# Performance work log

Measured on AMD Instinct MI355X. Metric: run time of the kernel, lower is better.

The kernel has to match this reference:

```python
import jax, jax.numpy as jnp
import numpy as np

A = 5          # angRes
C = 128        # channels
SPA = 2 * C    # spa_dim
NH = 8         # num_heads
KW = 11        # mask_field[1]


def setup_inputs() -> dict:
    key = jax.random.key(0)
    ks = jax.random.split(key, 12)
    s = 0.05
    return {
        "buffer": jax.random.normal(ks[0], (2, C, A * A, 32, 32), jnp.float32),
        "Win": jax.random.normal(ks[1], (SPA, C), jnp.float32) * s,
        "ln_w": jnp.ones((SPA,), jnp.float32),
        "ln_b": jnp.zeros((SPA,), jnp.float32),
        "in_proj": jax.random.normal(ks[2], (3 * SPA, SPA), jnp.float32) * s,
        "attn_out_w": jax.random.normal(ks[3], (SPA, SPA), jnp.float32) * s,
        "ffn_ln_w": jnp.ones((SPA,), jnp.float32),
        "ffn_ln_b": jnp.zeros((SPA,), jnp.float32),
        "ff1": jax.random.normal(ks[4], (2 * SPA, SPA), jnp.float32) * s,
        "ff2": jax.random.normal(ks[5], (SPA, 2 * SPA), jnp.float32) * s,
        "Wout": jax.random.normal(ks[6], (C, SPA), jnp.float32) * s,
        "conv_w": jax.random.normal(ks[7], (C, C, 1, 3, 3), jnp.float32) * s,
    }


def layer_norm(x, w, b, eps=1e-5):
    mu = x.mean(-1, keepdims=True)
    var = ((x - mu) ** 2).mean(-1, keepdims=True)
    return (x - mu) * jax.lax.rsqrt(var + eps) * w + b


def gen_mask(h, w, k_h, k_w):
    # additive mask over flattened (h*w) x (h*w) grid, local window k_h x k_w
    i = jnp.arange(h)
    j = jnp.arange(w)
    mh = (i[None, :] >= i[:, None] - k_h // 2) & (i[None, :] < i[:, None] + (k_h - k_h // 2))
    mw = (j[None, :] >= j[:, None] - k_w // 2) & (j[None, :] < j[:, None] + (k_w - k_w // 2))
    allowed = (mh[:, None, :, None] & mw[None, :, None, :]).reshape(h * w, h * w)
    return jnp.where(allowed, 0.0, -jnp.inf)


def basic_trans(x, Win, ln_w, ln_b, in_proj, attn_out_w,
                ffn_ln_w, ffn_ln_b, ff1, ff2, Wout):
    b, c, n, v, w = x.shape
    mask = gen_mask(v, w, 2 * A, KW)                       # (L, L)
    # 'b c n v w -> (v w) (b n) c'
    tok = x.transpose(3, 4, 0, 2, 1).reshape(v * w, b * n, c)
    tok = tok @ Win.T                                       # (L, B, E)
    tn = layer_norm(tok, ln_w, ln_b)
    L, B, E = tok.shape
    hd = E // NH
    Wq, Wk, Wv = jnp.split(in_proj, 3, axis=0)
    q = (tn @ Wq.T).reshape(L, B, NH, hd)
    k = (tn @ Wk.T).reshape(L, B, NH, hd)
    vv = (tok @ Wv.T).reshape(L, B, NH, hd)                 # value = un-normed tok
    scores = jnp.einsum('lbhd,mbhd->bhlm', q, k) / np.float32(np.sqrt(hd))
    scores = scores + mask[None, None]
    attn = jax.nn.softmax(scores, axis=-1)
    o = jnp.einsum('bhlm,mbhd->lbhd', attn, vv).reshape(L, B, E)
    tok = o @ attn_out_w.T + tok
    ff = layer_norm(tok, ffn_ln_w, ffn_ln_b)
    ff = jax.nn.relu(ff @ ff1.T) @ ff2.T
    tok = ff + tok
    tok = tok @ Wout.T                                      # (L, B, c)
    # '(v w) (b n) c -> b c n v w'
    return tok.reshape(v, w, b, n, c).transpose(2, 4, 3, 0, 1)


def reference(buffer, Win, ln_w, ln_b, in_proj, attn_out_w,
              ffn_ln_w, ffn_ln_b, ff1, ff2, Wout, conv_w):
    a = A
    b, c, uv, h, w = buffer.shape
    bt = lambda z: basic_trans(z, Win, ln_w, ln_b, in_proj, attn_out_w,
                               ffn_ln_w, ffn_ln_b, ff1, ff2, Wout)
    conv = lambda z: jax.lax.conv_general_dilated(
        z, conv_w, (1, 1, 1), ((0, 0), (1, 1), (1, 1)),
        dimension_numbers=('NCDHW', 'OIDHW', 'NCDHW'))

    # pass 1: 'b c (u v) h w -> b c (v w) u h'
    x = buffer.reshape(b, c, a, a, h, w).transpose(0, 1, 3, 5, 2, 4).reshape(b, c, a * w, a, h)
    x = bt(x)
    x = x.reshape(b, c, a, w, a, h).transpose(0, 1, 4, 2, 5, 3).reshape(b, c, a * a, h, w)
    x = conv(x) + buffer
    sc2 = x
    # pass 2: 'b c (u v) h w -> b c (u h) v w'
    y = x.reshape(b, c, a, a, h, w).transpose(0, 1, 2, 4, 3, 5).reshape(b, c, a * h, a, w)
    y = bt(y)
    y = y.reshape(b, c, a, h, a, w).transpose(0, 1, 2, 4, 3, 5).reshape(b, c, a * a, h, w)
    return conv(y) + sc2
```

## Files before the change

kernel.cpp:

```cpp
#include <hip/hip_runtime.h>
#include <math.h>
#include <stdint.h>

typedef __attribute__((ext_vector_type(8))) short bf16x8;
typedef __attribute__((ext_vector_type(4))) float f32x4;

static __device__ __forceinline__ unsigned short f2bf(float f) {
    unsigned u = __builtin_bit_cast(unsigned, f);
    unsigned r = u + 0x7fffu + ((u >> 16) & 1u);
    return (unsigned short)(r >> 16);
}
static __device__ __forceinline__ float bf2f(unsigned short h) {
    return __builtin_bit_cast(float, ((unsigned)h) << 16);
}
static __device__ __forceinline__ void gload_lds16(const void* g, void* l) {
    __builtin_amdgcn_global_load_lds((const __attribute__((address_space(1))) unsigned int*)g,
                                     (__attribute__((address_space(3))) unsigned int*)l, 16, 0, 0);
}

__global__ __launch_bounds__(256) void gather1(const float* __restrict__ src,
                                               unsigned short* __restrict__ x0, int W, int bb0) {
    int cct = blockIdx.x & 3, y = blockIdx.x >> 2;
    int n = blockIdx.y; int u = n / 5, v = n % 5;
    int lb = blockIdx.z, bb = bb0 + lb;
    __shared__ float tile[32][33];
    int tx = threadIdx.x & 31, tg = threadIdx.x >> 5;
    const float* s = src + (((size_t)(bb * 128 + cct * 32) * 25 + n) * 32 + y) * 32;
    #pragma unroll
    for (int i = 0; i < 4; i++) {
        int cl = tg + 8 * i;
        tile[cl][tx] = s[(size_t)cl * 25600 + tx];
    }
    __syncthreads();
    unsigned short* d = x0 + ((size_t)(u * 32 + y) * W + lb * 160 + v * 32) * 128 + cct * 32;
    #pragma unroll
    for (int i = 0; i < 4; i++) {
        int xx = tg + 8 * i;
        d[(size_t)xx * 128 + tx] = f2bf(tile[tx][xx]);
    }
}

__global__ __launch_bounds__(256) void gather2(const float* __restrict__ src,
                                               unsigned short* __restrict__ x0, int W, int bb0) {
    int cct = blockIdx.x & 3, x = blockIdx.x >> 2;
    int n = blockIdx.y; int u = n / 5, v = n % 5;
    int lb = blockIdx.z, bb = bb0 + lb;
    __shared__ float tile[32][33];
    int tx = threadIdx.x & 31, tg = threadIdx.x >> 5;
    const float* s = src + (((size_t)(bb * 128 + cct * 32) * 25 + n) * 32) * 32 + x;
    #pragma unroll
    for (int i = 0; i < 4; i++) {
        int cl = tg + 8 * i;
        tile[cl][tx] = s[(size_t)cl * 25600 + tx * 32];
    }
    __syncthreads();
    unsigned short* d = x0 + ((size_t)(v * 32 + x) * W + lb * 160 + u * 32) * 128 + cct * 32;
    #pragma unroll
    for (int i = 0; i < 4; i++) {
        int yy = tg + 8 * i;
        d[(size_t)yy * 128 + tx] = f2bf(tile[tx][yy]);
    }
}

__global__ __launch_bounds__(256) void repack_w(const float* __restrict__ cw,
                                                unsigned short* __restrict__ wb) {
    int g = blockIdx.x * 256 + threadIdx.x;
    int co = g / 1152;
    int rem = g - co * 1152;
    int ci = rem / 9, tap = rem - ci * 9;
    wb[((size_t)tap * 128 + co) * 128 + ci] = f2bf(cw[g]);
}

__global__ __launch_bounds__(256) void conv_weights(const float* __restrict__ Win,
                                                    const float* __restrict__ in_proj,
                                                    const float* __restrict__ attn_out_w,
                                                    const float* __restrict__ ff1,
                                                    const float* __restrict__ ff2,
                                                    const float* __restrict__ Wout,
                                                    unsigned short* __restrict__ wg) {
    int g = blockIdx.x * 256 + threadIdx.x;
    float v;
    if      (g < 32768)  v = Win[g];
    else if (g < 229376) v = in_proj[g - 32768];
    else if (g < 294912) v = attn_out_w[g - 229376];
    else if (g < 425984) v = ff1[g - 294912];
    else if (g < 557056) v = ff2[g - 425984];
    else                 v = Wout[g - 557056];
    wg[g] = f2bf(v);
}

__global__ __launch_bounds__(256) void ln_bf16(const unsigned short* __restrict__ in,
                                               unsigned short* __restrict__ out,
                                               const float* __restrict__ w, const float* __restrict__ b) {
    int tok = blockIdx.x * 4 + (threadIdx.x >> 6);
    int lane = threadIdx.x & 63;
    ushort4 h4 = ((const ushort4*)(in + (size_t)tok * 256))[lane];
    float vx = bf2f(h4.x), vy = bf2f(h4.y), vz = bf2f(h4.z), vw = bf2f(h4.w);
    float s = vx + vy + vz + vw;
    #pragma unroll
    for (int off = 32; off > 0; off >>= 1) s += __shfl_xor(s, off);
    float mu = s * (1.0f / 256.0f);
    float dx = vx - mu, dy = vy - mu, dz = vz - mu, dw = vw - mu;
    float vs = dx * dx + dy * dy + dz * dz + dw * dw;
    #pragma unroll
    for (int off = 32; off > 0; off >>= 1) vs += __shfl_xor(vs, off);
    float inv = rsqrtf(vs * (1.0f / 256.0f) + 1e-5f);
    float4 wv = ((const float4*)w)[lane];
    float4 bv = ((const float4*)b)[lane];
    ushort4 o4;
    o4.x = f2bf(dx * inv * wv.x + bv.x);
    o4.y = f2bf(dy * inv * wv.y + bv.y);
    o4.z = f2bf(dz * inv * wv.z + bv.z);
    o4.w = f2bf(dw * inv * wv.w + bv.w);
    *(ushort4*)(out + (size_t)tok * 256 + lane * 4) = o4;
}

static __device__ __forceinline__ void gemm_core(const unsigned short* __restrict__ X,
                                                 const unsigned short* __restrict__ Wt,
                                                 int bm, int bnrow, int K,
                                                 unsigned short (&As)[2][128 * 32],
                                                 unsigned short (&Bs)[2][128 * 32],
                                                 f32x4 (&acc)[4][4]) {
    const int tid = threadIdx.x;
    const int lane = tid & 63, w = tid >> 6;
    const int wm = (w >> 1) * 64, wn = (w & 1) * 64;
    const int lr = lane & 15, lq = lane >> 4;
    #pragma unroll
    for (int m = 0; m < 4; m++)
        #pragma unroll
        for (int n = 0; n < 4; n++)
            acc[m][n] = (f32x4){0.f, 0.f, 0.f, 0.f};

    const int srow = lane >> 2, sslot = lane & 3;
    auto STAGE = [&](int bsel, int k0) {
        #pragma unroll
        for (int c = 0; c < 2; ++c) {
            int row = (w << 5) + (c << 4) + srow;
            int sl = sslot ^ (row & 3);
            gload_lds16(X  + (size_t)(bm + row) * K + k0 + sl * 8,
                        &As[bsel][(w << 10) + (c << 9)]);
            gload_lds16(Wt + (size_t)(bnrow + row) * K + k0 + sl * 8,
                        &Bs[bsel][(w << 10) + (c << 9)]);
        }
    };

    const int nt = K >> 5;
    STAGE(0, 0);
    __syncthreads();
    int cur = 0;
    for (int t = 0; t < nt; ++t) {
        if (t + 1 < nt) STAGE(cur ^ 1, (t + 1) << 5);
        const char* Ab = (const char*)As[cur];
        const char* Bb = (const char*)Bs[cur];
        bf16x8 af[4], bf[4];
        #pragma unroll
        for (int m = 0; m < 4; m++) {
            int row = wm + m * 16 + lr;
            af[m] = *(const bf16x8*)(Ab + row * 64 + ((lq * 16) ^ ((row & 3) << 4)));
        }
        #pragma unroll
        for (int n = 0; n < 4; n++) {
            int row = wn + n * 16 + lr;
            bf[n] = *(const bf16x8*)(Bb + row * 64 + ((lq * 16) ^ ((row & 3) << 4)));
        }
        #pragma unroll
        for (int m = 0; m < 4; m++)
            #pragma unroll
            for (int n = 0; n < 4; n++)
                acc[m][n] = __builtin_amdgcn_mfma_f32_16x16x32_bf16(af[m], bf[n], acc[m][n], 0, 0, 0);
        if (t + 1 < nt) __syncthreads();
        cur ^= 1;
    }
}

__global__ __launch_bounds__(256) void gemm_bf16(const unsigned short* __restrict__ X,
                                                 const unsigned short* __restrict__ Wt,
                                                 unsigned short* __restrict__ Yb,
                                                 const unsigned short* __restrict__ Rb,
                                                 int N, int K, int relu, int spass, int W) {
    __shared__ unsigned short As[2][128 * 32];
    __shared__ unsigned short Bs[2][128 * 32];
    const int bm = blockIdx.x * 128, bn = blockIdx.y * 128;
    f32x4 acc[4][4];
    gemm_core(X, Wt, bm, bn, K, As, Bs, acc);

    const int lane = threadIdx.x & 63, w = threadIdx.x >> 6;
    const int wm = (w >> 1) * 64, wn = (w & 1) * 64;
    const int lr = lane & 15, lq = lane >> 4;
    #pragma unroll
    for (int m = 0; m < 4; m++) {
        #pragma unroll
        for (int r = 0; r < 4; r++) {
            int row = bm + wm + m * 16 + lq * 4 + r;
            size_t base;
            if (spass == 0) {
                base = (size_t)row * N;
            } else {
                int l = row / W, c = row - l * W;
                int lb = (c >= 160) ? 1 : 0, sp = c - lb * 160;
                int sl_, pix;
                if (spass == 1) { int u = l >> 5, y = l & 31, v = sp >> 5, x = sp & 31;
                                  sl_ = lb * 25 + u * 5 + v; pix = y * 32 + x; }
                else            { int v = l >> 5, x = l & 31, u = sp >> 5, y = sp & 31;
                                  sl_ = lb * 25 + u * 5 + v; pix = y * 32 + x; }
                base = ((size_t)sl_ * 1024 + pix) * 128;
            }
            #pragma unroll
            for (int n = 0; n < 4; n++) {
                int col = bn + wn + n * 16 + lr;
                float val = acc[m][n][r];
                if (Rb) val += bf2f(Rb[(size_t)row * N + col]);
                if (relu) val = fmaxf(val, 0.0f);
                Yb[base + col] = f2bf(val);
            }
        }
    }
}

__global__ __launch_bounds__(256) void gemm_qkv(const unsigned short* __restrict__ tn,
                                                const unsigned short* __restrict__ tok,
                                                const unsigned short* __restrict__ Wqkv,
                                                unsigned short* __restrict__ QK,
                                                unsigned short* __restrict__ V) {
    __shared__ unsigned short As[2][128 * 32];
    __shared__ unsigned short Bs[2][128 * 32];
    const int bm = blockIdx.x * 128, by = blockIdx.y;
    const unsigned short* X = (by < 4) ? tn : tok;
    f32x4 acc[4][4];
    gemm_core(X, Wqkv, bm, by * 128, 256, As, Bs, acc);

    unsigned short* Yb = (by < 4) ? QK : V;
    const int N = (by < 4) ? 512 : 256;
    const int bn = (by < 4) ? by * 128 : (by - 4) * 128;
    const int lane = threadIdx.x & 63, w = threadIdx.x >> 6;
    const int wm = (w >> 1) * 64, wn = (w & 1) * 64;
    const int lr = lane & 15, lq = lane >> 4;
    #pragma unroll
    for (int m = 0; m < 4; m++) {
        #pragma unroll
        for (int r = 0; r < 4; r++) {
            int row = bm + wm + m * 16 + lq * 4 + r;
            #pragma unroll
            for (int n = 0; n < 4; n++) {
                int col = bn + wn + n * 16 + lr;
                Yb[(size_t)row * N + col] = f2bf(acc[m][n][r]);
            }
        }
    }
}

__global__ __launch_bounds__(256) void vtrans(const unsigned short* __restrict__ vtok,
                                              unsigned short* __restrict__ vt, int W) {
    const int col = blockIdx.x, h = blockIdx.y;
    __shared__ unsigned short t[160][34];
    const int tid = threadIdx.x;
    for (int i = tid; i < 160 * 16; i += 256) {
        int l = i >> 4, dp = i & 15;
        unsigned v = *(const unsigned*)(vtok + ((size_t)l * W + col) * 256 + h * 32 + dp * 2);
        *(unsigned*)&t[l][dp * 2] = v;
    }
    __syncthreads();
    unsigned short* dst = vt + (((size_t)h * W + col) * 32) * 160;
    for (int i = tid; i < 32 * 160; i += 256) {
        int d = i / 160, l = i - d * 160;
        dst[i] = t[l][d];
    }
}

__global__ __launch_bounds__(64) void attn_mfma(const unsigned short* __restrict__ qk,
                                                const unsigned short* __restrict__ vt,
                                                unsigned short* __restrict__ o, int W) {
    const int col = blockIdx.x;
    const int h = blockIdx.y;
    const int lane = threadIdx.x;
    const int lr = lane & 15, lq = lane >> 4;
    __shared__ __align__(16) unsigned short P_lds[16][168];

    bf16x8 kf[10];
    #pragma unroll
    for (int m = 0; m < 10; m++) {
        size_t t = (size_t)(m * 16 + lr) * W + col;
        kf[m] = *(const bf16x8*)(qk + t * 512 + 256 + h * 32 + lq * 8);
    }
    const unsigned short* vbase = vt + (((size_t)h * W + col) * 32) * 160;
    bf16x8 vf[2][5];
    #pragma unroll
    for (int md = 0; md < 2; md++)
        #pragma unroll
        for (int c = 0; c < 5; c++)
            vf[md][c] = *(const bf16x8*)(vbase + (size_t)(md * 16 + lr) * 160 + c * 32 + lq * 8);

    const float scale = 0.17677669529663687f;
    for (int n = 0; n < 10; n++) {
        const int q = n * 16 + lr;
        bf16x8 qf = *(const bf16x8*)(qk + ((size_t)q * W + col) * 512 + h * 32 + lq * 8);
        f32x4 p[10];
        #pragma unroll
        for (int m = 0; m < 10; m++)
            p[m] = __builtin_amdgcn_mfma_f32_16x16x32_bf16(kf[m], qf, (f32x4){0.f,0.f,0.f,0.f}, 0, 0, 0);
        const int b = lq * 4 - ((n & 1) * 16 + lr);
        float mx = -1e30f;
        #pragma unroll
        for (int m = 0; m < 10; m++) {
            #pragma unroll
            for (int r = 0; r < 4; r++) {
                int dd = b + (m & 1) * 16 + r;
                float s = ((unsigned)(dd + 5) <= 10u) ? p[m][r] : -1e30f;
                p[m][r] = s;
                mx = fmaxf(mx, s);
            }
        }
        mx = fmaxf(mx, __shfl_xor(mx, 16));
        mx = fmaxf(mx, __shfl_xor(mx, 32));
        float sum = 0.f;
        #pragma unroll
        for (int m = 0; m < 10; m++) {
            #pragma unroll
            for (int r = 0; r < 4; r++) {
                float e = __expf((p[m][r] - mx) * scale);
                p[m][r] = e;
                sum += e;
            }
        }
        sum += __shfl_xor(sum, 16);
        sum += __shfl_xor(sum, 32);
        #pragma unroll
        for (int m = 0; m < 10; m++) {
            ushort4 pk;
            pk.x = f2bf(p[m][0]); pk.y = f2bf(p[m][1]);
            pk.z = f2bf(p[m][2]); pk.w = f2bf(p[m][3]);
            *(ushort4*)&P_lds[lr][m * 16 + lq * 4] = pk;
        }
        f32x4 oa0 = (f32x4){0.f,0.f,0.f,0.f}, oa1 = (f32x4){0.f,0.f,0.f,0.f};
        #pragma unroll
        for (int c = 0; c < 5; c++) {
            bf16x8 pf = *(const bf16x8*)&P_lds[lr][c * 32 + lq * 8];
            oa0 = __builtin_amdgcn_mfma_f32_16x16x32_bf16(vf[0][c], pf, oa0, 0, 0, 0);
            oa1 = __builtin_amdgcn_mfma_f32_16x16x32_bf16(vf[1][c], pf, oa1, 0, 0, 0);
        }
        const float inv = 1.0f / sum;
        unsigned short* op = o + ((size_t)q * W + col) * 256 + h * 32;
        ushort4 s0, s1;
        s0.x = f2bf(oa0[0] * inv); s0.y = f2bf(oa0[1] * inv);
        s0.z = f2bf(oa0[2] * inv); s0.w = f2bf(oa0[3] * inv);
        s1.x = f2bf(oa1[0] * inv); s1.y = f2bf(oa1[1] * inv);
        s1.z = f2bf(oa1[2] * inv); s1.w = f2bf(oa1[3] * inv);
        *(ushort4*)(op + lq * 4)      = s0;
        *(ushort4*)(op + 16 + lq * 4) = s1;
    }
}

__global__ __launch_bounds__(256) void conv_mfma(const unsigned short* __restrict__ xp,
                                                 const unsigned short* __restrict__ wb,
                                                 const float* __restrict__ res,
                                                 float* __restrict__ out, int bb0) {
    const int ptile = blockIdx.x;
    const int slice = blockIdx.y;
    const int lb = slice / 25, n = slice % 25;
    const int bb = bb0 + lb;
    const int y0 = ptile * 4;
    __shared__ unsigned short As[128 * 64];
    __shared__ unsigned short Bs[128 * 64];
    const int tid = threadIdx.x;
    const int lane = tid & 63, w = tid >> 6;
    const int wm = (w >> 1) * 64;
    const int wn = (w & 1) * 64;
    const int lr = lane & 15, lq = lane >> 4;
    const unsigned short* xs = xp + (size_t)slice * 1024 * 128;
    f32x4 acc[4][4];
    #pragma unroll
    for (int m = 0; m < 4; m++)
        #pragma unroll
        for (int nn = 0; nn < 4; nn++)
            acc[m][nn] = (f32x4){0.f, 0.f, 0.f, 0.f};

    for (int tap = 0; tap < 9; tap++) {
        const int dy = tap / 3 - 1, dx = tap % 3 - 1;
        for (int c0 = 0; c0 < 128; c0 += 64) {
            #pragma unroll
            for (int i = 0; i < 4; i++) {
                int id = tid + 256 * i;
                int row = id >> 3, cg = id & 7;
                int py = y0 + (row >> 5) + dy;
                int px = (row & 31) + dx;
                uint4 v = {0u, 0u, 0u, 0u};
                if ((unsigned)py < 32u && (unsigned)px < 32u)
                    v = *(const uint4*)(xs + ((size_t)(py * 32 + px) * 128 + c0 + cg * 8));
                int boff = row * 128 + ((cg * 16) ^ ((row & 7) << 4));
                *(uint4*)((char*)As + boff) = v;
            }
            #pragma unroll
            for (int i = 0; i < 4; i++) {
                int id = tid + 256 * i;
                int row = id >> 3, cg = id & 7;
                uint4 v = *(const uint4*)(wb + (((size_t)tap * 128 + row) * 128 + c0 + cg * 8));
                int boff = row * 128 + ((cg * 16) ^ ((row & 7) << 4));
                *(uint4*)((char*)Bs + boff) = v;
            }
            __syncthreads();
            #pragma unroll
            for (int ks = 0; ks < 2; ks++) {
                bf16x8 wf[4], xf[4];
                #pragma unroll
                for (int m = 0; m < 4; m++) {
                    int row = wm + m * 16 + lr;
                    int boff = row * 128 + ((ks * 64 + lq * 16) ^ ((row & 7) << 4));
                    wf[m] = *(const bf16x8*)((const char*)Bs + boff);
                }
                #pragma unroll
                for (int nn = 0; nn < 4; nn++) {
                    int row = wn + nn * 16 + lr;
                    int boff = row * 128 + ((ks * 64 + lq * 16) ^ ((row & 7) << 4));
                    xf[nn] = *(const bf16x8*)((const char*)As + boff);
                }
                #pragma unroll
                for (int m = 0; m < 4; m++)
                    #pragma unroll
                    for (int nn = 0; nn < 4; nn++)
                        acc[m][nn] = __builtin_amdgcn_mfma_f32_16x16x32_bf16(wf[m], xf[nn], acc[m][nn], 0, 0, 0);
            }
            __syncthreads();
        }
    }
    #pragma unroll
    for (int m = 0; m < 4; m++) {
        int co0 = wm + m * 16 + lq * 4;
        #pragma unroll
        for (int r = 0; r < 4; r++) {
            size_t rowoff = (((size_t)(bb * 128 + co0 + r) * 25 + n) * 1024) + ptile * 128;
            #pragma unroll
            for (int nn = 0; nn < 4; nn++) {
                int pix = wn + nn * 16 + lr;
                out[rowoff + pix] = acc[m][nn][r] + res[rowoff + pix];
            }
        }
    }
}

extern "C" void kernel_launch(void* const* d_in, const int* in_sizes, int n_in,
                              void* d_out, int out_size, void* d_ws, size_t ws_size,
                              hipStream_t stream) {
    (void)in_sizes; (void)n_in; (void)out_size;
    const float* buffer     = (const float*)d_in[0];
    const float* Win        = (const float*)d_in[1];
    const float* ln_w       = (const float*)d_in[2];
    const float* ln_b       = (const float*)d_in[3];
    const float* in_proj    = (const float*)d_in[4];
    const float* attn_out_w = (const float*)d_in[5];
    const float* ffn_ln_w   = (const float*)d_in[6];
    const float* ffn_ln_b   = (const float*)d_in[7];
    const float* ff1        = (const float*)d_in[8];
    const float* ff2        = (const float*)d_in[9];
    const float* Wout       = (const float*)d_in[10];
    const float* conv_w     = (const float*)d_in[11];
    float* out = (float*)d_out;
    float* ws  = (float*)d_ws;

    const size_t need2 = ((size_t)51200 * 960 + 368640) * 4;
    int NBB = (ws_size >= need2) ? 2 : 1;
    const int W = NBB * 160;
    const size_t T = (size_t)NBB * 25600;

    unsigned short* x0b   = (unsigned short*)ws;
    unsigned short* Abf   = (unsigned short*)(ws + T * 64);
    unsigned short* tnb   = (unsigned short*)(ws + T * 192);
    float*          C     = ws + T * 320;
    unsigned short* QKtok = (unsigned short*)C;
    unsigned short* Vtok  = (unsigned short*)(C + T * 256);
    unsigned short* Vt    = (unsigned short*)(C + T * 384);
    unsigned short* hidb  = (unsigned short*)C;
    unsigned short* xp    = (unsigned short*)C;
    unsigned short* Db    = (unsigned short*)(ws + T * 832);
    unsigned short* wg    = (unsigned short*)(ws + T * 960);
    unsigned short* wb    = (unsigned short*)(ws + T * 960 + 294912);

    const unsigned short* Winb  = wg;
    const unsigned short* Wqkvb = wg + 32768;
    const unsigned short* Waob  = wg + 229376;
    const unsigned short* Wff1b = wg + 294912;
    const unsigned short* Wff2b = wg + 425984;
    const unsigned short* Woutb = wg + 557056;

    const int GM = (int)(T / 128);

    conv_weights<<<2304, 256, 0, stream>>>(Win, in_proj, attn_out_w, ff1, ff2, Wout, wg);
    repack_w<<<576, 256, 0, stream>>>(conv_w, wb);

    for (int pass = 0; pass < 2; pass++) {
        const float* src = (pass == 0) ? buffer : out;
        for (int bb0 = 0; bb0 < 2; bb0 += NBB) {
            if (pass == 0) gather1<<<dim3(128, 25, NBB), 256, 0, stream>>>(src, x0b, W, bb0);
            else           gather2<<<dim3(128, 25, NBB), 256, 0, stream>>>(src, x0b, W, bb0);

            gemm_bf16<<<dim3(GM, 2), 256, 0, stream>>>(x0b, Winb, Abf, nullptr, 256, 128, 0, 0, W);
            ln_bf16<<<(int)(T / 4), 256, 0, stream>>>(Abf, tnb, ln_w, ln_b);
            gemm_qkv<<<dim3(GM, 6), 256, 0, stream>>>(tnb, Abf, Wqkvb, QKtok, Vtok);
            vtrans<<<dim3(W, 8), 256, 0, stream>>>(Vtok, Vt, W);
            attn_mfma<<<dim3(W, 8), 64, 0, stream>>>(QKtok, Vt, Db, W);
            gemm_bf16<<<dim3(GM, 2), 256, 0, stream>>>(Db, Waob, Abf, Abf, 256, 256, 0, 0, W);
            ln_bf16<<<(int)(T / 4), 256, 0, stream>>>(Abf, tnb, ffn_ln_w, ffn_ln_b);
            gemm_bf16<<<dim3(GM, 4), 256, 0, stream>>>(tnb, Wff1b, hidb, nullptr, 512, 256, 1, 0, W);
            gemm_bf16<<<dim3(GM, 2), 256, 0, stream>>>(hidb, Wff2b, Abf, Abf, 256, 512, 0, 0, W);
            gemm_bf16<<<dim3(GM, 1), 256, 0, stream>>>(Abf, Woutb, xp, nullptr, 128, 256, 0, pass + 1, W);

            conv_mfma<<<dim3(8, NBB * 25), 256, 0, stream>>>(
                xp, wb, (pass == 0) ? buffer : (const float*)out, out, bb0);
        }
    }
}
```

Baseline: 658.6 us.

## Triple-buffer GEMM LDS staging and fuse V transpose into QKV epilogue

The shared GEMM core moves from double to triple buffering. It issues loads two k-tiles ahead and waits with explicit vmcnt counters plus raw barriers instead of __syncthreads. The LDS swizzle pattern changes from row&3 to (row>>1)&3 to cut bank conflicts on the fragment reads. The separate vtrans kernel is removed: the QKV GEMM epilogue writes V straight into the transposed per-head layout. That saves one launch and one round trip of V through memory, at the cost of scattered 2-byte stores and more LDS per block, which may lower occupancy.

```diff
diff --git a/kernel.cpp b/kernel.cpp
--- a/kernel.cpp
+++ b/kernel.cpp
@@ -118,8 +118,8 @@
 static __device__ __forceinline__ void gemm_core(const unsigned short* __restrict__ X,
                                                  const unsigned short* __restrict__ Wt,
                                                  int bm, int bnrow, int K,
-                                                 unsigned short (&As)[2][128 * 32],
-                                                 unsigned short (&Bs)[2][128 * 32],
+                                                 unsigned short (&As)[3][128 * 32],
+                                                 unsigned short (&Bs)[3][128 * 32],
                                                  f32x4 (&acc)[4][4]) {
     const int tid = threadIdx.x;
     const int lane = tid & 63, w = tid >> 6;
@@ -136,7 +136,7 @@
         #pragma unroll
         for (int c = 0; c < 2; ++c) {
             int row = (w << 5) + (c << 4) + srow;
-            int sl = sslot ^ (row & 3);
+            int sl = sslot ^ ((row >> 1) & 3);
             gload_lds16(X  + (size_t)(bm + row) * K + k0 + sl * 8,
                         &As[bsel][(w << 10) + (c << 9)]);
             gload_lds16(Wt + (size_t)(bnrow + row) * K + k0 + sl * 8,
@@ -146,30 +146,36 @@
 
     const int nt = K >> 5;
     STAGE(0, 0);
-    __syncthreads();
-    int cur = 0;
+    STAGE(1, 32);
+    asm volatile("s_waitcnt vmcnt(4)" ::: "memory");
+    __builtin_amdgcn_s_barrier();
+    __builtin_amdgcn_sched_barrier(0);
     for (int t = 0; t < nt; ++t) {
-        if (t + 1 < nt) STAGE(cur ^ 1, (t + 1) << 5);
-        const char* Ab = (const char*)As[cur];
-        const char* Bb = (const char*)Bs[cur];
+        if (t + 2 < nt) STAGE((t + 2) % 3, (t + 2) << 5);
+        const char* Ab = (const char*)As[t % 3];
+        const char* Bb = (const char*)Bs[t % 3];
         bf16x8 af[4], bf[4];
         #pragma unroll
         for (int m = 0; m < 4; m++) {
             int row = wm + m * 16 + lr;
-            af[m] = *(const bf16x8*)(Ab + row * 64 + ((lq * 16) ^ ((row & 3) << 4)));
+            af[m] = *(const bf16x8*)(Ab + row * 64 + ((lq * 16) ^ (((row >> 1) & 3) << 4)));
         }
         #pragma unroll
         for (int n = 0; n < 4; n++) {
             int row = wn + n * 16 + lr;
-            bf[n] = *(const bf16x8*)(Bb + row * 64 + ((lq * 16) ^ ((row & 3) << 4)));
+            bf[n] = *(const bf16x8*)(Bb + row * 64 + ((lq * 16) ^ (((row >> 1) & 3) << 4)));
         }
         #pragma unroll
         for (int m = 0; m < 4; m++)
             #pragma unroll
             for (int n = 0; n < 4; n++)
                 acc[m][n] = __builtin_amdgcn_mfma_f32_16x16x32_bf16(af[m], bf[n], acc[m][n], 0, 0, 0);
-        if (t + 1 < nt) __syncthreads();
-        cur ^= 1;
+        if (t + 1 < nt) {
+            if (t + 2 < nt) asm volatile("s_waitcnt vmcnt(4)" ::: "memory");
+            else            asm volatile("s_waitcnt vmcnt(0)" ::: "memory");
+            __builtin_amdgcn_s_barrier();
+            __builtin_amdgcn_sched_barrier(0);
+        }
     }
 }
 
@@ -178,8 +184,8 @@
                                                  unsigned short* __restrict__ Yb,
                                                  const unsigned short* __restrict__ Rb,
                                                  int N, int K, int relu, int spass, int W) {
-    __shared__ unsigned short As[2][128 * 32];
-    __shared__ unsigned short Bs[2][128 * 32];
+    __shared__ unsigned short As[3][128 * 32];
+    __shared__ unsigned short Bs[3][128 * 32];
     const int bm = blockIdx.x * 128, bn = blockIdx.y * 128;
     f32x4 acc[4][4];
     gemm_core(X, Wt, bm, bn, K, As, Bs, acc);
@@ -221,49 +227,46 @@
                                                 const unsigned short* __restrict__ tok,
                                                 const unsigned short* __restrict__ Wqkv,
                                                 unsigned short* __restrict__ QK,
-                                                unsigned short* __restrict__ V) {
-    __shared__ unsigned short As[2][128 * 32];
-    __shared__ unsigned short Bs[2][128 * 32];
+                                                unsigned short* __restrict__ Vt, int W) {
+    __shared__ unsigned short As[3][128 * 32];
+    __shared__ unsigned short Bs[3][128 * 32];
     const int bm = blockIdx.x * 128, by = blockIdx.y;
     const unsigned short* X = (by < 4) ? tn : tok;
     f32x4 acc[4][4];
     gemm_core(X, Wqkv, bm, by * 128, 256, As, Bs, acc);
 
-    unsigned short* Yb = (by < 4) ? QK : V;
-    const int N = (by < 4) ? 512 : 256;
-    const int bn = (by < 4) ? by * 128 : (by - 4) * 128;
     const int lane = threadIdx.x & 63, w = threadIdx.x >> 6;
     const int wm = (w >> 1) * 64, wn = (w & 1) * 64;
     const int lr = lane & 15, lq = lane >> 4;
-    #pragma unroll
-    for (int m = 0; m < 4; m++) {
-        #pragma unroll
-        for (int r = 0; r < 4; r++) {
-            int row = bm + wm + m * 16 + lq * 4 + r;
-            #pragma unroll
-            for (int n = 0; n < 4; n++) {
-                int col = bn + wn + n * 16 + lr;
-                Yb[(size_t)row * N + col] = f2bf(acc[m][n][r]);
-            }
-        }
-    }
-}
-
-__global__ __launch_bounds__(256) void vtrans(const unsigned short* __restrict__ vtok,
-                                              unsigned short* __restrict__ vt, int W) {
-    const int col = blockIdx.x, h = blockIdx.y;
-    __shared__ unsigned short t[160][34];
-    const int tid = threadIdx.x;
-    for (int i = tid; i < 160 * 16; i += 256) {
-        int l = i >> 4, dp = i & 15;
-        unsigned v = *(const unsigned*)(vtok + ((size_t)l * W + col) * 256 + h * 32 + dp * 2);
-        *(unsigned*)&t[l][dp * 2] = v;
-    }
-    __syncthreads();
-    unsigned short* dst = vt + (((size_t)h * W + col) * 32) * 160;
-    for (int i = tid; i < 32 * 160; i += 256) {
-        int d = i / 160, l = i - d * 160;
-        dst[i] = t[l][d];
+    if (by < 4) {
+        const int bn = by * 128;
+        #pragma unroll
+        for (int m = 0; m < 4; m++) {
+            #pragma unroll
+            for (int r = 0; r < 4; r++) {
+                int row = bm + wm + m * 16 + lq * 4 + r;
+                #pragma unroll
+                for (int n = 0; n < 4; n++) {
+                    int col = bn + wn + n * 16 + lr;
+                    QK[(size_t)row * 512 + col] = f2bf(acc[m][n][r]);
+                }
+            }
+        }
+    } else {
+        #pragma unroll
+        for (int m = 0; m < 4; m++) {
+            #pragma unroll
+            for (int r = 0; r < 4; r++) {
+                int row = bm + wm + m * 16 + lq * 4 + r;
+                int l = row / W, c = row - l * W;
+                #pragma unroll
+                for (int n = 0; n < 4; n++) {
+                    int vr = (by - 4) * 128 + wn + n * 16 + lr;
+                    int h = vr >> 5, d = vr & 31;
+                    Vt[(((size_t)h * W + c) * 32 + d) * 160 + l] = f2bf(acc[m][n][r]);
+                }
+            }
+        }
     }
 }
 
@@ -466,7 +469,6 @@
     unsigned short* tnb   = (unsigned short*)(ws + T * 192);
     float*          C     = ws + T * 320;
     unsigned short* QKtok = (unsigned short*)C;
-    unsigned short* Vtok  = (unsigned short*)(C + T * 256);
     unsigned short* Vt    = (unsigned short*)(C + T * 384);
     unsigned short* hidb  = (unsigned short*)C;
     unsigned short* xp    = (unsigned short*)C;
@@ -494,8 +496,7 @@
 
             gemm_bf16<<<dim3(GM, 2), 256, 0, stream>>>(x0b, Winb, Abf, nullptr, 256, 128, 0, 0, W);
             ln_bf16<<<(int)(T / 4), 256, 0, stream>>>(Abf, tnb, ln_w, ln_b);
-            gemm_qkv<<<dim3(GM, 6), 256, 0, stream>>>(tnb, Abf, Wqkvb, QKtok, Vtok);
-            vtrans<<<dim3(W, 8), 256, 0, stream>>>(Vtok, Vt, W);
+            gemm_qkv<<<dim3(GM, 6), 256, 0, stream>>>(tnb, Abf, Wqkvb, QKtok, Vt, W);
             attn_mfma<<<dim3(W, 8), 64, 0, stream>>>(QKtok, Vt, Db, W);
             gemm_bf16<<<dim3(GM, 2), 256, 0, stream>>>(Db, Waob, Abf, Abf, 256, 256, 0, 0, W);
             ln_bf16<<<(int)(T / 4), 256, 0, stream>>>(Abf, tnb, ffn_ln_w, ffn_ln_b);
```

New measurement: 807.1 us. +22.6%, slower.

## Shrink GEMM tiles to 64x64 and remap blocks across XCDs

Applied to the files above, without the earlier changes.

Replaces the 128x128 GEMM tile core with a 64x64 variant, where each wave computes a 32x32 sub-tile and all 256 threads issue one LDS load each per operand. The LDS swizzle pattern is adjusted to match. A block-index remap groups consecutive M tiles onto the same XCD so they share L2 reuse of the weights and activations. Grids grow fourfold to give the 256 CUs more blocks to keep busy. The cost is less data reuse per block and lower MFMA density per wave.

```diff
diff --git a/kernel.cpp b/kernel.cpp
--- a/kernel.cpp
+++ b/kernel.cpp
@@ -115,33 +115,39 @@
     *(ushort4*)(out + (size_t)tok * 256 + lane * 4) = o4;
 }
 
-static __device__ __forceinline__ void gemm_core(const unsigned short* __restrict__ X,
-                                                 const unsigned short* __restrict__ Wt,
-                                                 int bm, int bnrow, int K,
-                                                 unsigned short (&As)[2][128 * 32],
-                                                 unsigned short (&Bs)[2][128 * 32],
-                                                 f32x4 (&acc)[4][4]) {
+static __device__ __forceinline__ void xcd_remap(int& bxi, int& byi) {
+    int d = blockIdx.x + gridDim.x * blockIdx.y;
+    int s = d & 7;
+    unsigned j = (unsigned)(d >> 3);
+    unsigned ny = gridDim.y;
+    int gm8 = (int)(gridDim.x >> 3);
+    bxi = s * gm8 + (int)(j / ny);
+    byi = (int)(j % ny);
+}
+
+static __device__ __forceinline__ void gemm_core64(const unsigned short* __restrict__ X,
+                                                   const unsigned short* __restrict__ Wt,
+                                                   int bm, int bnrow, int K,
+                                                   unsigned short (&As)[2][64 * 32],
+                                                   unsigned short (&Bs)[2][64 * 32],
+                                                   f32x4 (&acc)[2][2]) {
     const int tid = threadIdx.x;
     const int lane = tid & 63, w = tid >> 6;
-    const int wm = (w >> 1) * 64, wn = (w & 1) * 64;
+    const int wm = (w >> 1) * 32, wn = (w & 1) * 32;
     const int lr = lane & 15, lq = lane >> 4;
     #pragma unroll
-    for (int m = 0; m < 4; m++)
-        #pragma unroll
-        for (int n = 0; n < 4; n++)
+    for (int m = 0; m < 2; m++)
+        #pragma unroll
+        for (int n = 0; n < 2; n++)
             acc[m][n] = (f32x4){0.f, 0.f, 0.f, 0.f};
 
-    const int srow = lane >> 2, sslot = lane & 3;
+    const int srow = tid >> 2, sslot = tid & 3;
+    const int ssl = sslot ^ ((srow >> 1) & 3);
     auto STAGE = [&](int bsel, int k0) {
-        #pragma unroll
-        for (int c = 0; c < 2; ++c) {
-            int row = (w << 5) + (c << 4) + srow;
-            int sl = sslot ^ (row & 3);
-            gload_lds16(X  + (size_t)(bm + row) * K + k0 + sl * 8,
-                        &As[bsel][(w << 10) + (c << 9)]);
-            gload_lds16(Wt + (size_t)(bnrow + row) * K + k0 + sl * 8,
-                        &Bs[bsel][(w << 10) + (c << 9)]);
-        }
+        gload_lds16(X  + (size_t)(bm + srow) * K + k0 + ssl * 8,
+                    &As[bsel][tid * 8]);
+        gload_lds16(Wt + (size_t)(bnrow + srow) * K + k0 + ssl * 8,
+                    &Bs[bsel][tid * 8]);
     };
 
     const int nt = K >> 5;
@@ -152,21 +158,21 @@
         if (t + 1 < nt) STAGE(cur ^ 1, (t + 1) << 5);
         const char* Ab = (const char*)As[cur];
         const char* Bb = (const char*)Bs[cur];
-        bf16x8 af[4], bf[4];
-        #pragma unroll
-        for (int m = 0; m < 4; m++) {
+        bf16x8 af[2], bf[2];
+        #pragma unroll
+        for (int m = 0; m < 2; m++) {
             int row = wm + m * 16 + lr;
-            af[m] = *(const bf16x8*)(Ab + row * 64 + ((lq * 16) ^ ((row & 3) << 4)));
-        }
-        #pragma unroll
-        for (int n = 0; n < 4; n++) {
+            af[m] = *(const bf16x8*)(Ab + row * 64 + ((lq * 16) ^ (((row >> 1) & 3) << 4)));
+        }
+        #pragma unroll
+        for (int n = 0; n < 2; n++) {
             int row = wn + n * 16 + lr;
-            bf[n] = *(const bf16x8*)(Bb + row * 64 + ((lq * 16) ^ ((row & 3) << 4)));
-        }
-        #pragma unroll
-        for (int m = 0; m < 4; m++)
-            #pragma unroll
-            for (int n = 0; n < 4; n++)
+            bf[n] = *(const bf16x8*)(Bb + row * 64 + ((lq * 16) ^ (((row >> 1) & 3) << 4)));
+        }
+        #pragma unroll
+        for (int m = 0; m < 2; m++)
+            #pragma unroll
+            for (int n = 0; n < 2; n++)
                 acc[m][n] = __builtin_amdgcn_mfma_f32_16x16x32_bf16(af[m], bf[n], acc[m][n], 0, 0, 0);
         if (t + 1 < nt) __syncthreads();
         cur ^= 1;
@@ -178,17 +184,19 @@
                                                  unsigned short* __restrict__ Yb,
                                                  const unsigned short* __restrict__ Rb,
                                                  int N, int K, int relu, int spass, int W) {
-    __shared__ unsigned short As[2][128 * 32];
-    __shared__ unsigned short Bs[2][128 * 32];
-    const int bm = blockIdx.x * 128, bn = blockIdx.y * 128;
-    f32x4 acc[4][4];
-    gemm_core(X, Wt, bm, bn, K, As, Bs, acc);
+    __shared__ unsigned short As[2][64 * 32];
+    __shared__ unsigned short Bs[2][64 * 32];
+    int bxi, byi;
+    xcd_remap(bxi, byi);
+    const int bm = bxi * 64, bn = byi * 64;
+    f32x4 acc[2][2];
+    gemm_core64(X, Wt, bm, bn, K, As, Bs, acc);
 
     const int lane = threadIdx.x & 63, w = threadIdx.x >> 6;
-    const int wm = (w >> 1) * 64, wn = (w & 1) * 64;
+    const int wm = (w >> 1) * 32, wn = (w & 1) * 32;
     const int lr = lane & 15, lq = lane >> 4;
     #pragma unroll
-    for (int m = 0; m < 4; m++) {
+    for (int m = 0; m < 2; m++) {
         #pragma unroll
         for (int r = 0; r < 4; r++) {
             int row = bm + wm + m * 16 + lq * 4 + r;
@@ -206,7 +214,7 @@
                 base = ((size_t)sl_ * 1024 + pix) * 128;
             }
             #pragma unroll
-            for (int n = 0; n < 4; n++) {
+            for (int n = 0; n < 2; n++) {
                 int col = bn + wn + n * 16 + lr;
                 float val = acc[m][n][r];
                 if (Rb) val += bf2f(Rb[(size_t)row * N + col]);
@@ -222,26 +230,28 @@
                                                 const unsigned short* __restrict__ Wqkv,
                                                 unsigned short* __restrict__ QK,
                                                 unsigned short* __restrict__ V) {
-    __shared__ unsigned short As[2][128 * 32];
-    __shared__ unsigned short Bs[2][128 * 32];
-    const int bm = blockIdx.x * 128, by = blockIdx.y;
-    const unsigned short* X = (by < 4) ? tn : tok;
-    f32x4 acc[4][4];
-    gemm_core(X, Wqkv, bm, by * 128, 256, As, Bs, acc);
-
-    unsigned short* Yb = (by < 4) ? QK : V;
-    const int N = (by < 4) ? 512 : 256;
-    const int bn = (by < 4) ? by * 128 : (by - 4) * 128;
+    __shared__ unsigned short As[2][64 * 32];
+    __shared__ unsigned short Bs[2][64 * 32];
+    int bxi, by;
+    xcd_remap(bxi, by);
+    const int bm = bxi * 64;
+    const unsigned short* X = (by < 8) ? tn : tok;
+    f32x4 acc[2][2];
+    gemm_core64(X, Wqkv, bm, by * 64, 256, As, Bs, acc);
+
+    unsigned short* Yb = (by < 8) ? QK : V;
+    const int N = (by < 8) ? 512 : 256;
+    const int bn = (by < 8) ? by * 64 : (by - 8) * 64;
     const int lane = threadIdx.x & 63, w = threadIdx.x >> 6;
-    const int wm = (w >> 1) * 64, wn = (w & 1) * 64;
+    const int wm = (w >> 1) * 32, wn = (w & 1) * 32;
     const int lr = lane & 15, lq = lane >> 4;
     #pragma unroll
-    for (int m = 0; m < 4; m++) {
+    for (int m = 0; m < 2; m++) {
         #pragma unroll
         for (int r = 0; r < 4; r++) {
             int row = bm + wm + m * 16 + lq * 4 + r;
             #pragma unroll
-            for (int n = 0; n < 4; n++) {
+            for (int n = 0; n < 2; n++) {
                 int col = bn + wn + n * 16 + lr;
                 Yb[(size_t)row * N + col] = f2bf(acc[m][n][r]);
             }
@@ -481,7 +491,7 @@
     const unsigned short* Wff2b = wg + 425984;
     const unsigned short* Woutb = wg + 557056;
 
-    const int GM = (int)(T / 128);
+    const int GM64 = (int)(T / 64);
 
     conv_weights<<<2304, 256, 0, stream>>>(Win, in_proj, attn_out_w, ff1, ff2, Wout, wg);
     repack_w<<<576, 256, 0, stream>>>(conv_w, wb);
@@ -492,16 +502,16 @@
             if (pass == 0) gather1<<<dim3(128, 25, NBB), 256, 0, stream>>>(src, x0b, W, bb0);
             else           gather2<<<dim3(128, 25, NBB), 256, 0, stream>>>(src, x0b, W, bb0);
 
-            gemm_bf16<<<dim3(GM, 2), 256, 0, stream>>>(x0b, Winb, Abf, nullptr, 256, 128, 0, 0, W);
+            gemm_bf16<<<dim3(GM64, 4), 256, 0, stream>>>(x0b, Winb, Abf, nullptr, 256, 128, 0, 0, W);
             ln_bf16<<<(int)(T / 4), 256, 0, stream>>>(Abf, tnb, ln_w, ln_b);
-            gemm_qkv<<<dim3(GM, 6), 256, 0, stream>>>(tnb, Abf, Wqkvb, QKtok, Vtok);
+            gemm_qkv<<<dim3(GM64, 12), 256, 0, stream>>>(tnb, Abf, Wqkvb, QKtok, Vtok);
             vtrans<<<dim3(W, 8), 256, 0, stream>>>(Vtok, Vt, W);
             attn_mfma<<<dim3(W, 8), 64, 0, stream>>>(QKtok, Vt, Db, W);
-            gemm_bf16<<<dim3(GM, 2), 256, 0, stream>>>(Db, Waob, Abf, Abf, 256, 256, 0, 0, W);
+            gemm_bf16<<<dim3(GM64, 4), 256, 0, stream>>>(Db, Waob, Abf, Abf, 256, 256, 0, 0, W);
             ln_bf16<<<(int)(T / 4), 256, 0, stream>>>(Abf, tnb, ffn_ln_w, ffn_ln_b);
-            gemm_bf16<<<dim3(GM, 4), 256, 0, stream>>>(tnb, Wff1b, hidb, nullptr, 512, 256, 1, 0, W);
-            gemm_bf16<<<dim3(GM, 2), 256, 0, stream>>>(hidb, Wff2b, Abf, Abf, 256, 512, 0, 0, W);
-            gemm_bf16<<<dim3(GM, 1), 256, 0, stream>>>(Abf, Woutb, xp, nullptr, 128, 256, 0, pass + 1, W);
+            gemm_bf16<<<dim3(GM64, 8), 256, 0, stream>>>(tnb, Wff1b, hidb, nullptr, 512, 256, 1, 0, W);
+            gemm_bf16<<<dim3(GM64, 4), 256, 0, stream>>>(hidb, Wff2b, Abf, Abf, 256, 512, 0, 0, W);
+            gemm_bf16<<<dim3(GM64, 2), 256, 0, stream>>>(Abf, Woutb, xp, nullptr, 128, 256, 0, pass + 1, W);
 
             conv_mfma<<<dim3(8, NBB * 25), 256, 0, stream>>>(
                 xp, wb, (pass == 0) ? buffer : (const float*)out, out, bb0);
```

Measured after the change: 593.2 us. 1.11x faster.
